# Optimization experiments

Measured on AMD Instinct MI355X. Metric: run time of the kernel, lower is better.

Reference implementation:

```python
import jax, jax.numpy as jnp
import numpy as np

B, L, D, H, R = 2, 2048, 1024, 16, 32
DH = D // H
LORA_SCALE = 64.0 / 32.0  # alpha / rank


def _ln(x, w, b):
    mu = jnp.mean(x, axis=-1, keepdims=True)
    xc = x - mu
    var = jnp.mean(xc * xc, axis=-1, keepdims=True)
    y = xc * jax.lax.rsqrt(var + 1e-5) * w
    return y + b if b is not None else y


def _rotate_half(x):
    x1, x2 = jnp.split(x, 2, axis=-1)
    return jnp.concatenate([-x2, x1], axis=-1)


def _apply_rotary(q, k):
    # q, k: [B, L, H, DH]
    seqlen = q.shape[1]
    inv_freq = 1.0 / (10000.0 ** (jnp.arange(0, DH, 2, dtype=jnp.float32) / DH))
    t = jnp.arange(seqlen, dtype=jnp.float32)
    freqs = t[:, None] * inv_freq[None, :]           # [L, DH/2]
    emb = jnp.concatenate([freqs, freqs], axis=-1)   # [L, DH]
    cos = jnp.cos(emb)[None, :, None, :]
    sin = jnp.sin(emb)[None, :, None, :]
    q = q * cos + _rotate_half(q) * sin
    k = k * cos + _rotate_half(k) * sin
    return q, k


def setup_inputs() -> dict:
    key = jax.random.key(0)
    ks = jax.random.split(key, 10)
    s = 0.02
    return {
        "x": jax.random.normal(ks[0], (B, L, D), dtype=jnp.float32),
        "seq_id": jnp.sort(jax.random.randint(ks[1], (B, L), 0, 4), axis=-1),
        "ln_w": jnp.ones((D,), jnp.float32),
        "ln_b": jnp.zeros((D,), jnp.float32),
        "w_qkv": jax.random.normal(ks[2], (3 * D, D), jnp.float32) * s,
        "q_lora_a": jax.random.normal(ks[3], (R, D), jnp.float32) * s,
        "q_lora_b": jax.random.normal(ks[4], (D, R), jnp.float32) * s,
        "v_lora_a": jax.random.normal(ks[5], (R, D), jnp.float32) * s,
        "v_lora_b": jax.random.normal(ks[6], (D, R), jnp.float32) * s,
        "q_ln_w": jnp.ones((D,), jnp.float32),
        "k_ln_w": jnp.ones((D,), jnp.float32),
        "w_out": jax.random.normal(ks[7], (D, D), jnp.float32) * s,
    }


def reference(x, seq_id, ln_w, ln_b, w_qkv, q_lora_a, q_lora_b,
              v_lora_a, v_lora_b, q_ln_w, k_ln_w, w_out):
    h = _ln(x, ln_w, ln_b)                          # [B, L, D]
    qkv = jnp.einsum('bld,ed->ble', h, w_qkv)       # [B, L, 3D]
    q, k, v = jnp.split(qkv, 3, axis=-1)
    q = q + LORA_SCALE * jnp.einsum('blr,dr->bld', jnp.einsum('bld,rd->blr', h, q_lora_a), q_lora_b)
    v = v + LORA_SCALE * jnp.einsum('blr,dr->bld', jnp.einsum('bld,rd->blr', h, v_lora_a), v_lora_b)
    q = _ln(q, q_ln_w, None)
    k = _ln(k, k_ln_w, None)
    q = q.reshape(B, L, H, DH)
    k = k.reshape(B, L, H, DH)
    q, k = _apply_rotary(q, k)
    qh = q.transpose(0, 2, 1, 3)                    # [B, H, L, DH]
    kh = k.transpose(0, 2, 1, 3)
    vh = v.reshape(B, L, H, DH).transpose(0, 2, 1, 3)
    scale = 1.0 / np.sqrt(DH)
    scores = jnp.einsum('bhqd,bhkd->bhqk', qh, kh) * scale
    mask = (seq_id[:, None, :, None] == seq_id[:, None, None, :])  # [B,1,L,L]
    scores = jnp.where(mask, scores, jnp.finfo(scores.dtype).min)
    attn = jax.nn.softmax(scores, axis=-1)
    ctx = jnp.einsum('bhqk,bhkd->bhqd', attn, vh)   # [B, H, L, DH]
    ctx = ctx.transpose(0, 2, 1, 3).reshape(B, L, D)
    return jnp.einsum('bld,ed->ble', ctx, w_out)
```

## Files before the change

kernel.cpp:

```cpp
#include <hip/hip_runtime.h>
#include <hip/hip_bf16.h>
#include <cmath>

constexpr int Bb = 2;
constexpr int Ls = 2048;
constexpr int Dd = 1024;
constexpr int Hh = 16;
constexpr int DHh = 64;
constexpr int Rr = 32;
constexpr int BL = Bb * Ls;
constexpr float LORA_SCALE = 2.0f;
constexpr float LN_EPS = 1e-5f;
constexpr float ATTN_SCALE = 0.125f;
constexpr float LOG2E = 1.4426950408889634f;
constexpr float QSCL = ATTN_SCALE * LOG2E;

typedef __attribute__((ext_vector_type(8))) short bf16x8;
typedef __attribute__((ext_vector_type(4))) float f32x4;

__device__ __forceinline__ unsigned short f2bf(float f) {
    __hip_bfloat16 b = __float2bfloat16(f);
    return *reinterpret_cast<unsigned short*>(&b);
}
__device__ __forceinline__ float bf2f(unsigned short u) {
    unsigned int x = ((unsigned int)u) << 16;
    return __uint_as_float(x);
}
__device__ __forceinline__ void async_copy16(const void* g, void* l) {
    __builtin_amdgcn_global_load_lds(
        (__attribute__((address_space(1))) void*)(void*)(size_t)g,
        (__attribute__((address_space(3))) void*)l, 16, 0, 0);
}

__device__ __forceinline__ float block_sum_256(float v, float* red) {
#pragma unroll
    for (int o = 32; o > 0; o >>= 1) v += __shfl_down(v, o, 64);
    const int lane = threadIdx.x & 63;
    const int wid = threadIdx.x >> 6;
    if (lane == 0) red[wid] = v;
    __syncthreads();
    float s = red[0] + red[1] + red[2] + red[3];
    __syncthreads();
    return s;
}

__global__ __launch_bounds__(256) void prep_ln_kernel(const float* __restrict__ w,
                                                      const float* __restrict__ qa,
                                                      const float* __restrict__ qb,
                                                      const float* __restrict__ va,
                                                      const float* __restrict__ vb,
                                                      const float* __restrict__ wout,
                                                      const float* __restrict__ x,
                                                      const float* __restrict__ lnw,
                                                      const float* __restrict__ lnb,
                                                      unsigned short* __restrict__ wqkvb,
                                                      unsigned short* __restrict__ woutb,
                                                      float* __restrict__ ropec,
                                                      float* __restrict__ ropes,
                                                      unsigned short* __restrict__ hb) {
    const int blk = blockIdx.x;
    const int tid = threadIdx.x;
    if (blk < 3 * Dd) {
        const int e = blk;
        const int d0 = tid * 4;
        __shared__ float br[Rr];
        const bool isq = (e < Dd);
        const bool isv = (e >= 2 * Dd);
        const float* bsrc = isq ? (qb + (size_t)e * Rr)
                                : (isv ? (vb + (size_t)(e - 2 * Dd) * Rr) : nullptr);
        const float* asrc = isq ? qa : va;
        if (bsrc && tid < Rr) br[tid] = bsrc[tid];
        __syncthreads();
        float acc[4] = {0.f, 0.f, 0.f, 0.f};
        if (bsrc) {
#pragma unroll 8
            for (int r = 0; r < Rr; ++r) {
                float4 av = *(const float4*)(asrc + (size_t)r * Dd + d0);
                acc[0] += br[r] * av.x; acc[1] += br[r] * av.y;
                acc[2] += br[r] * av.z; acc[3] += br[r] * av.w;
            }
        }
        float4 wv = *(const float4*)(w + (size_t)e * Dd + d0);
        ushort4 o;
        o.x = f2bf(wv.x + LORA_SCALE * acc[0]);
        o.y = f2bf(wv.y + LORA_SCALE * acc[1]);
        o.z = f2bf(wv.z + LORA_SCALE * acc[2]);
        o.w = f2bf(wv.w + LORA_SCALE * acc[3]);
        *(ushort4*)(wqkvb + (size_t)e * Dd + d0) = o;
    } else if (blk < 4 * Dd) {
        int i = ((blk - 3 * Dd) * 256 + tid) * 4;
        float4 v = *(const float4*)(wout + i);
        ushort4 o;
        o.x = f2bf(v.x); o.y = f2bf(v.y); o.z = f2bf(v.z); o.w = f2bf(v.w);
        *(ushort4*)(woutb + i) = o;
    } else if (blk < 4 * Dd + 256) {
        int i = (blk - 4 * Dd) * 256 + tid;
        int l = i >> 5;
        int f = i & 31;
        float invf = powf(10000.0f, -(float)f * (1.0f / 32.0f));
        float ang = (float)l * invf;
        float s, c;
        sincosf(ang, &s, &c);
        ropec[i] = c;
        ropes[i] = s;
    } else {
        const int w64 = tid >> 6;
        const int L = tid & 63;
        const int row = (blk - (4 * Dd + 256)) * 4 + w64;
        const float* xr = x + (size_t)row * Dd;
        float4 v4[4];
        float v[16];
#pragma unroll
        for (int c = 0; c < 4; ++c) {
            v4[c] = *(const float4*)(xr + c * 256 + L * 4);
            v[c * 4 + 0] = v4[c].x; v[c * 4 + 1] = v4[c].y;
            v[c * 4 + 2] = v4[c].z; v[c * 4 + 3] = v4[c].w;
        }
        float s = 0.f;
#pragma unroll
        for (int j = 0; j < 16; ++j) s += v[j];
#pragma unroll
        for (int off = 1; off < 64; off <<= 1) s += __shfl_xor(s, off, 64);
        float mean = s * (1.0f / Dd);
        float sq = 0.f;
#pragma unroll
        for (int j = 0; j < 16; ++j) {
            v[j] -= mean;
            sq += v[j] * v[j];
        }
#pragma unroll
        for (int off = 1; off < 64; off <<= 1) sq += __shfl_xor(sq, off, 64);
        float rs = rsqrtf(sq * (1.0f / Dd) + LN_EPS);
        unsigned short* hr = hb + (size_t)row * Dd;
#pragma unroll
        for (int c = 0; c < 4; ++c) {
            int d = c * 256 + L * 4;
            float4 wv = *(const float4*)(lnw + d);
            float4 bv = *(const float4*)(lnb + d);
            ushort4 o;
            o.x = f2bf(v[c * 4 + 0] * rs * wv.x + bv.x);
            o.y = f2bf(v[c * 4 + 1] * rs * wv.y + bv.y);
            o.z = f2bf(v[c * 4 + 2] * rs * wv.z + bv.z);
            o.w = f2bf(v[c * 4 + 3] * rs * wv.w + bv.w);
            *(ushort4*)(hr + d) = o;
        }
    }
}

__global__ __launch_bounds__(256) void gemm_bt_mfma(const unsigned short* __restrict__ A,
                                                    const unsigned short* __restrict__ B,
                                                    unsigned short* __restrict__ C,
                                                    int M, int N, int K) {
    __shared__ short As[128 * 64];
    __shared__ short Bs[128 * 64];
    const int tid = threadIdx.x;
    const int w = tid >> 6, lane = tid & 63, quad = lane >> 4, l15 = lane & 15;
    const int m0 = blockIdx.y * 128, n0 = blockIdx.x * 128;
    const int wm = (w & 1) * 64, wn = (w >> 1) * 64;
    f32x4 acc[4][4];
#pragma unroll
    for (int i = 0; i < 4; ++i)
#pragma unroll
        for (int j = 0; j < 4; ++j) acc[i][j] = f32x4{0.f, 0.f, 0.f, 0.f};

    for (int k0 = 0; k0 < K; k0 += 64) {
#pragma unroll
        for (int j = 0; j < 4; ++j) {
            int c = tid + j * 256;
            int row = c >> 3;
            int jg = (c & 7) ^ (row & 7);
            async_copy16(A + (size_t)(m0 + row) * K + k0 + jg * 8, As + c * 8);
        }
#pragma unroll
        for (int j = 0; j < 4; ++j) {
            int c = tid + j * 256;
            int row = c >> 3;
            int jg = (c & 7) ^ (row & 7);
            async_copy16(B + (size_t)(n0 + row) * K + k0 + jg * 8, Bs + c * 8);
        }
        __syncthreads();
#pragma unroll
        for (int ks = 0; ks < 2; ++ks) {
            bf16x8 a[4], b[4];
#pragma unroll
            for (int mi = 0; mi < 4; ++mi) {
                int row = wm + mi * 16 + l15;
                int ch = (ks * 4 + quad) ^ (row & 7);
                a[mi] = *(const bf16x8*)&As[row * 64 + ch * 8];
            }
#pragma unroll
            for (int ni = 0; ni < 4; ++ni) {
                int row = wn + ni * 16 + l15;
                int ch = (ks * 4 + quad) ^ (row & 7);
                b[ni] = *(const bf16x8*)&Bs[row * 64 + ch * 8];
            }
#pragma unroll
            for (int mi = 0; mi < 4; ++mi)
#pragma unroll
                for (int ni = 0; ni < 4; ++ni)
                    acc[mi][ni] = __builtin_amdgcn_mfma_f32_16x16x32_bf16(a[mi], b[ni], acc[mi][ni], 0, 0, 0);
        }
        __syncthreads();
    }
#pragma unroll
    for (int mi = 0; mi < 4; ++mi)
#pragma unroll
        for (int ni = 0; ni < 4; ++ni)
#pragma unroll
            for (int r = 0; r < 4; ++r)
                C[(size_t)(m0 + wm + mi * 16 + quad * 4 + r) * N + n0 + wn + ni * 16 + l15] =
                    f2bf(acc[mi][ni][r]);
}

__global__ __launch_bounds__(256) void gemm_bt_mfma_n64(const unsigned short* __restrict__ A,
                                                        const unsigned short* __restrict__ B,
                                                        float* __restrict__ C,
                                                        int M, int N, int K) {
    __shared__ short As[128 * 64];
    __shared__ short Bs[64 * 64];
    const int tid = threadIdx.x;
    const int w = tid >> 6, lane = tid & 63, quad = lane >> 4, l15 = lane & 15;
    const int m0 = blockIdx.y * 128, n0 = blockIdx.x * 64;
    const int wm = (w & 1) * 64, wn = (w >> 1) * 32;
    f32x4 acc[4][2];
#pragma unroll
    for (int i = 0; i < 4; ++i)
#pragma unroll
        for (int j = 0; j < 2; ++j) acc[i][j] = f32x4{0.f, 0.f, 0.f, 0.f};

    for (int k0 = 0; k0 < K; k0 += 64) {
#pragma unroll
        for (int j = 0; j < 4; ++j) {
            int c = tid + j * 256;
            int row = c >> 3;
            int jg = (c & 7) ^ (row & 7);
            async_copy16(A + (size_t)(m0 + row) * K + k0 + jg * 8, As + c * 8);
        }
#pragma unroll
        for (int j = 0; j < 2; ++j) {
            int c = tid + j * 256;
            int row = c >> 3;
            int jg = (c & 7) ^ (row & 7);
            async_copy16(B + (size_t)(n0 + row) * K + k0 + jg * 8, Bs + c * 8);
        }
        __syncthreads();
#pragma unroll
        for (int ks = 0; ks < 2; ++ks) {
            bf16x8 a[4], b[2];
#pragma unroll
            for (int mi = 0; mi < 4; ++mi) {
                int row = wm + mi * 16 + l15;
                int ch = (ks * 4 + quad) ^ (row & 7);
                a[mi] = *(const bf16x8*)&As[row * 64 + ch * 8];
            }
#pragma unroll
            for (int ni = 0; ni < 2; ++ni) {
                int row = wn + ni * 16 + l15;
                int ch = (ks * 4 + quad) ^ (row & 7);
                b[ni] = *(const bf16x8*)&Bs[row * 64 + ch * 8];
            }
#pragma unroll
            for (int mi = 0; mi < 4; ++mi)
#pragma unroll
                for (int ni = 0; ni < 2; ++ni)
                    acc[mi][ni] = __builtin_amdgcn_mfma_f32_16x16x32_bf16(a[mi], b[ni], acc[mi][ni], 0, 0, 0);
        }
        __syncthreads();
    }
#pragma unroll
    for (int mi = 0; mi < 4; ++mi)
#pragma unroll
        for (int ni = 0; ni < 2; ++ni)
#pragma unroll
            for (int r = 0; r < 4; ++r)
                C[(size_t)(m0 + wm + mi * 16 + quad * 4 + r) * N + n0 + wn + ni * 16 + l15] =
                    acc[mi][ni][r];
}

__global__ __launch_bounds__(256) void qkv_final_kernel(const unsigned short* __restrict__ qkvb,
                                                        const float* __restrict__ qlnw,
                                                        const float* __restrict__ klnw,
                                                        const float* __restrict__ ropec,
                                                        const float* __restrict__ ropes,
                                                        unsigned short* __restrict__ qt,
                                                        unsigned short* __restrict__ kt,
                                                        unsigned short* __restrict__ vtt) {
    const int blk = blockIdx.x;
    const int tid = threadIdx.x;
    if (blk < BL / 4) {
        const int w64 = tid >> 6;
        const int L = tid & 63;
        const int row = blk * 4 + w64;
        const int b = row >> 11;
        const int l = row & (Ls - 1);
        const unsigned short* qp = qkvb + (size_t)row * (3 * Dd);
        const unsigned short* kp = qp + Dd;

        bf16x8 qA = *(const bf16x8*)(qp + L * 8);
        bf16x8 qB = *(const bf16x8*)(qp + 512 + L * 8);
        bf16x8 kA = *(const bf16x8*)(kp + L * 8);
        bf16x8 kB = *(const bf16x8*)(kp + 512 + L * 8);
        float vq[16], vk[16];
#pragma unroll
        for (int j = 0; j < 8; ++j) {
            vq[j] = bf2f((unsigned short)qA[j]);
            vq[8 + j] = bf2f((unsigned short)qB[j]);
            vk[j] = bf2f((unsigned short)kA[j]);
            vk[8 + j] = bf2f((unsigned short)kB[j]);
        }
        float sq = 0.f, sk = 0.f;
#pragma unroll
        for (int j = 0; j < 16; ++j) { sq += vq[j]; sk += vk[j]; }
#pragma unroll
        for (int off = 1; off < 64; off <<= 1) {
            sq += __shfl_xor(sq, off, 64);
            sk += __shfl_xor(sk, off, 64);
        }
        float mq = sq * (1.0f / Dd), mk = sk * (1.0f / Dd);
        float vvq = 0.f, vvk = 0.f;
#pragma unroll
        for (int j = 0; j < 16; ++j) {
            vq[j] -= mq; vvq += vq[j] * vq[j];
            vk[j] -= mk; vvk += vk[j] * vk[j];
        }
#pragma unroll
        for (int off = 1; off < 64; off <<= 1) {
            vvq += __shfl_xor(vvq, off, 64);
            vvk += __shfl_xor(vvk, off, 64);
        }
        float rsq = rsqrtf(vvq * (1.0f / Dd) + LN_EPS);
        float rsk = rsqrtf(vvk * (1.0f / Dd) + LN_EPS);

        float yq[16], yk[16];
        {
            float4 w0 = *(const float4*)(qlnw + L * 8);
            float4 w1 = *(const float4*)(qlnw + L * 8 + 4);
            float4 w2 = *(const float4*)(qlnw + 512 + L * 8);
            float4 w3 = *(const float4*)(qlnw + 512 + L * 8 + 4);
            const float* wp = (const float*)&w0;
            yq[0] = vq[0] * rsq * w0.x; yq[1] = vq[1] * rsq * w0.y;
            yq[2] = vq[2] * rsq * w0.z; yq[3] = vq[3] * rsq * w0.w;
            yq[4] = vq[4] * rsq * w1.x; yq[5] = vq[5] * rsq * w1.y;
            yq[6] = vq[6] * rsq * w1.z; yq[7] = vq[7] * rsq * w1.w;
            yq[8] = vq[8] * rsq * w2.x; yq[9] = vq[9] * rsq * w2.y;
            yq[10] = vq[10] * rsq * w2.z; yq[11] = vq[11] * rsq * w2.w;
            yq[12] = vq[12] * rsq * w3.x; yq[13] = vq[13] * rsq * w3.y;
            yq[14] = vq[14] * rsq * w3.z; yq[15] = vq[15] * rsq * w3.w;
            (void)wp;
        }
        {
            float4 w0 = *(const float4*)(klnw + L * 8);
            float4 w1 = *(const float4*)(klnw + L * 8 + 4);
            float4 w2 = *(const float4*)(klnw + 512 + L * 8);
            float4 w3 = *(const float4*)(klnw + 512 + L * 8 + 4);
            yk[0] = vk[0] * rsk * w0.x; yk[1] = vk[1] * rsk * w0.y;
            yk[2] = vk[2] * rsk * w0.z; yk[3] = vk[3] * rsk * w0.w;
            yk[4] = vk[4] * rsk * w1.x; yk[5] = vk[5] * rsk * w1.y;
            yk[6] = vk[6] * rsk * w1.z; yk[7] = vk[7] * rsk * w1.w;
            yk[8] = vk[8] * rsk * w2.x; yk[9] = vk[9] * rsk * w2.y;
            yk[10] = vk[10] * rsk * w2.z; yk[11] = vk[11] * rsk * w2.w;
            yk[12] = vk[12] * rsk * w3.x; yk[13] = vk[13] * rsk * w3.y;
            yk[14] = vk[14] * rsk * w3.z; yk[15] = vk[15] * rsk * w3.w;
        }

        float cs[8], sn[8];
        {
            int fbase = l * 32 + (L & 3) * 8;
            float4 c0 = *(const float4*)(ropec + fbase);
            float4 c1 = *(const float4*)(ropec + fbase + 4);
            float4 s0 = *(const float4*)(ropes + fbase);
            float4 s1 = *(const float4*)(ropes + fbase + 4);
            cs[0] = c0.x; cs[1] = c0.y; cs[2] = c0.z; cs[3] = c0.w;
            cs[4] = c1.x; cs[5] = c1.y; cs[6] = c1.z; cs[7] = c1.w;
            sn[0] = s0.x; sn[1] = s0.y; sn[2] = s0.z; sn[3] = s0.w;
            sn[4] = s1.x; sn[5] = s1.y; sn[6] = s1.z; sn[7] = s1.w;
        }
        const float sgn = (L & 4) ? 1.0f : -1.0f;
        ushort4 oqA0, oqA1, oqB0, oqB1, okA0, okA1, okB0, okB1;
        unsigned short* pqA = (unsigned short*)&oqA0;
        unsigned short outqA[8], outqB[8], outkA[8], outkB[8];
#pragma unroll
        for (int j = 0; j < 8; ++j) {
            float pA = __shfl_xor(yq[j], 4, 64);
            float pB = __shfl_xor(yq[8 + j], 4, 64);
            outqA[j] = f2bf((yq[j] * cs[j] + sgn * pA * sn[j]) * QSCL);
            outqB[j] = f2bf((yq[8 + j] * cs[j] + sgn * pB * sn[j]) * QSCL);
            float pkA = __shfl_xor(yk[j], 4, 64);
            float pkB = __shfl_xor(yk[8 + j], 4, 64);
            outkA[j] = f2bf(yk[j] * cs[j] + sgn * pkA * sn[j]);
            outkB[j] = f2bf(yk[8 + j] * cs[j] + sgn * pkB * sn[j]);
        }
        (void)pqA; (void)oqA1; (void)oqB0; (void)oqB1; (void)okA0; (void)okA1; (void)okB0; (void)okB1;
        const int hA = L >> 3;
        const int dh0 = (L & 7) * 8;
        size_t offA = (((size_t)(b * Hh + hA)) * Ls + l) * DHh + dh0;
        size_t offB = (((size_t)(b * Hh + 8 + hA)) * Ls + l) * DHh + dh0;
        *(uint4*)(qt + offA) = *(uint4*)outqA;
        *(uint4*)(qt + offB) = *(uint4*)outqB;
        *(uint4*)(kt + offA) = *(uint4*)outkA;
        *(uint4*)(kt + offB) = *(uint4*)outkB;
    } else {
        const int t2 = blk - BL / 4;
        const int l0 = (t2 & 31) * 64;
        const int h = (t2 >> 5) & 15;
        const int b = t2 >> 9;
        __shared__ short t[64][72];
        const unsigned short* src = qkvb + (size_t)b * Ls * (3 * Dd) + 2 * Dd + h * 64;
#pragma unroll
        for (int j = 0; j < 2; ++j) {
            int g = tid + j * 256;
            int row = g >> 3;
            int c0 = (g & 7) * 8;
            uint4 vv = *(const uint4*)(src + (size_t)(l0 + row) * (3 * Dd) + c0);
            *(uint4*)&t[row][c0] = vv;
        }
        __syncthreads();
        unsigned short* dst = vtt + ((size_t)(b * Hh + h) * DHh) * Ls;
#pragma unroll
        for (int j = 0; j < 2; ++j) {
            int g = tid + j * 256;
            int dh = g >> 3;
            int lc = (g & 7) * 8;
            ushort4 o0, o1;
            unsigned short* p0 = (unsigned short*)&o0;
            unsigned short* p1 = (unsigned short*)&o1;
#pragma unroll
            for (int i = 0; i < 4; ++i) p0[i] = (unsigned short)t[lc + i][dh];
#pragma unroll
            for (int i = 0; i < 4; ++i) p1[i] = (unsigned short)t[lc + 4 + i][dh];
            *(ushort4*)(dst + (size_t)dh * Ls + l0 + lc) = o0;
            *(ushort4*)(dst + (size_t)dh * Ls + l0 + lc + 4) = o1;
        }
    }
}

constexpr int PSP = 76;

__global__ __launch_bounds__(256) void attn_kernel(const unsigned short* __restrict__ qt,
                                                   const unsigned short* __restrict__ kt,
                                                   const unsigned short* __restrict__ vtt,
                                                   const int* __restrict__ seq_id,
                                                   unsigned short* __restrict__ ctxb) {
    const int id = blockIdx.x;
    const int c8 = id & 7;
    const int x = (id >> 3) & 15;
    const int g4 = id >> 7;
    const int v = c8 + 8 * g4;
    const int b = v >> 4;
    const int h = v & 15;
    const int q0 = x * 128;

    const size_t base = ((size_t)(b * Hh + h)) * Ls * DHh;
    const size_t base_v = ((size_t)(b * Hh + h)) * DHh * Ls;
    const int* sid = seq_id + (size_t)b * Ls;

    __shared__ short Ks[64 * 64];
    __shared__ short Vs[64 * 64];
    __shared__ short Ps[8][16 * PSP];
    __shared__ int sq_s[128];

    const int tid = threadIdx.x;
    const int w = tid >> 6;
    const int lane = tid & 63;
    const int quad = lane >> 4;
    const int l15 = lane & 15;

    if (tid < 128) sq_s[tid] = sid[q0 + tid];
    const int qmin = sid[q0];
    const int qmax = sid[q0 + 127];

    bf16x8 a0[2], a1[2];
#pragma unroll
    for (int sub = 0; sub < 2; ++sub) {
        int qrow = q0 + sub * 64 + w * 16 + l15;
        a0[sub] = *(const bf16x8*)(qt + base + (size_t)qrow * DHh + quad * 8);
        a1[sub] = *(const bf16x8*)(qt + base + (size_t)qrow * DHh + 32 + quad * 8);
    }

    bool need = false;
    if (lane < 32) {
        int kmn = sid[lane * 64];
        int kmx = sid[lane * 64 + 63];
        need = (kmn <= qmax) && (kmx >= qmin);
    }
    unsigned long long bmask = __ballot(need);
    const int t0 = __builtin_ctzll(bmask);
    const int t1 = 64 - __builtin_clzll(bmask);

    float lsum[2][4] = {{0.f, 0.f, 0.f, 0.f}, {0.f, 0.f, 0.f, 0.f}};
    f32x4 O[2][4];
#pragma unroll
    for (int sub = 0; sub < 2; ++sub)
#pragma unroll
        for (int r = 0; r < 4; ++r) O[sub][r] = f32x4{0.f, 0.f, 0.f, 0.f};

    for (int t = t0; t < t1; ++t) {
        const int k0 = t * 64;
        __syncthreads();
#pragma unroll
        for (int j = 0; j < 2; ++j) {
            int cc = tid + j * 256;
            int row = cc >> 3;
            int jg = (cc & 7) ^ (row & 7);
            async_copy16(kt + base + (size_t)(k0 + row) * DHh + jg * 8, &Ks[cc * 8]);
            async_copy16(vtt + base_v + (size_t)row * Ls + k0 + jg * 8, &Vs[cc * 8]);
        }
        __syncthreads();

        f32x4 s[2][4];
#pragma unroll
        for (int kg = 0; kg < 4; ++kg) {
            int krow = kg * 16 + l15;
            bf16x8 b0 = *(const bf16x8*)&Ks[krow * 64 + ((0 + quad) ^ (krow & 7)) * 8];
            bf16x8 b1 = *(const bf16x8*)&Ks[krow * 64 + ((4 + quad) ^ (krow & 7)) * 8];
#pragma unroll
            for (int sub = 0; sub < 2; ++sub) {
                f32x4 acc = {0.f, 0.f, 0.f, 0.f};
                acc = __builtin_amdgcn_mfma_f32_16x16x32_bf16(a0[sub], b0, acc, 0, 0, 0);
                acc = __builtin_amdgcn_mfma_f32_16x16x32_bf16(a1[sub], b1, acc, 0, 0, 0);
                s[sub][kg] = acc;
            }
        }
        const int kmn = sid[k0];
        const int kmx = sid[k0 + 63];
        const bool nomask = (kmn == kmx) && (qmin == qmax) && (kmn == qmin);
        if (!nomask) {
#pragma unroll
            for (int sub = 0; sub < 2; ++sub) {
                int sqv[4];
#pragma unroll
                for (int r = 0; r < 4; ++r) sqv[r] = sq_s[sub * 64 + w * 16 + quad * 4 + r];
#pragma unroll
                for (int kg = 0; kg < 4; ++kg) {
                    int skv = sid[k0 + kg * 16 + l15];
#pragma unroll
                    for (int r = 0; r < 4; ++r)
                        if (sqv[r] != skv) s[sub][kg][r] = -3.0e38f;
                }
            }
        }
#pragma unroll
        for (int sub = 0; sub < 2; ++sub) {
#pragma unroll
            for (int kg = 0; kg < 4; ++kg)
#pragma unroll
                for (int r = 0; r < 4; ++r)
                    s[sub][kg][r] = __builtin_amdgcn_exp2f(s[sub][kg][r]);
#pragma unroll
            for (int r = 0; r < 4; ++r)
                lsum[sub][r] += s[sub][0][r] + s[sub][1][r] + s[sub][2][r] + s[sub][3][r];
#pragma unroll
            for (int kg = 0; kg < 4; ++kg)
#pragma unroll
                for (int r = 0; r < 4; ++r)
                    Ps[w * 2 + sub][(quad * 4 + r) * PSP + kg * 16 + l15] =
                        (short)f2bf(s[sub][kg][r]);
        }
        bf16x8 pa0[2], pa1[2];
#pragma unroll
        for (int sub = 0; sub < 2; ++sub) {
            pa0[sub] = *(const bf16x8*)&Ps[w * 2 + sub][l15 * PSP + quad * 8];
            pa1[sub] = *(const bf16x8*)&Ps[w * 2 + sub][l15 * PSP + 32 + quad * 8];
        }
#pragma unroll
        for (int ng = 0; ng < 4; ++ng) {
            int vrow = ng * 16 + l15;
            bf16x8 vb0 = *(const bf16x8*)&Vs[vrow * 64 + ((0 + quad) ^ (vrow & 7)) * 8];
            bf16x8 vb1 = *(const bf16x8*)&Vs[vrow * 64 + ((4 + quad) ^ (vrow & 7)) * 8];
#pragma unroll
            for (int sub = 0; sub < 2; ++sub) {
                O[sub][ng] = __builtin_amdgcn_mfma_f32_16x16x32_bf16(pa0[sub], vb0, O[sub][ng], 0, 0, 0);
                O[sub][ng] = __builtin_amdgcn_mfma_f32_16x16x32_bf16(pa1[sub], vb1, O[sub][ng], 0, 0, 0);
            }
        }
    }

#pragma unroll
    for (int sub = 0; sub < 2; ++sub) {
#pragma unroll
        for (int off = 1; off < 16; off <<= 1)
#pragma unroll
            for (int r = 0; r < 4; ++r)
                lsum[sub][r] += __shfl_xor(lsum[sub][r], off, 64);
        float inv_l[4];
#pragma unroll
        for (int r = 0; r < 4; ++r) inv_l[r] = 1.0f / lsum[sub][r];
#pragma unroll
        for (int ng = 0; ng < 4; ++ng)
#pragma unroll
            for (int r = 0; r < 4; ++r) {
                int q = q0 + sub * 64 + w * 16 + quad * 4 + r;
                ctxb[((size_t)b * Ls + q) * Dd + h * DHh + ng * 16 + l15] =
                    f2bf(O[sub][ng][r] * inv_l[r]);
            }
    }
}

extern "C" void kernel_launch(void* const* d_in, const int* in_sizes, int n_in,
                              void* d_out, int out_size, void* d_ws, size_t ws_size,
                              hipStream_t stream) {
    const float* x = (const float*)d_in[0];
    const int* seq_id = (const int*)d_in[1];
    const float* ln_w = (const float*)d_in[2];
    const float* ln_b = (const float*)d_in[3];
    const float* w_qkv = (const float*)d_in[4];
    const float* q_lora_a = (const float*)d_in[5];
    const float* q_lora_b = (const float*)d_in[6];
    const float* v_lora_a = (const float*)d_in[7];
    const float* v_lora_b = (const float*)d_in[8];
    const float* q_ln_w = (const float*)d_in[9];
    const float* k_ln_w = (const float*)d_in[10];
    const float* w_out = (const float*)d_in[11];
    float* out = (float*)d_out;

    const size_t SZ = (size_t)BL * Dd;
    float* p = (float*)d_ws;
    float* ropec = p;          p += (size_t)Ls * 32;
    float* ropes = p;          p += (size_t)Ls * 32;
    unsigned short* ub = (unsigned short*)p;
    unsigned short* qkvb = ub; ub += 3 * SZ;
    unsigned short* hb = ub;   ub += SZ;
    unsigned short* qt = ub;   ub += SZ;
    unsigned short* kt = ub;   ub += SZ;
    unsigned short* vtt = ub;  ub += SZ;
    unsigned short* ctxb = ub; ub += SZ;
    unsigned short* wqkvb = ub; ub += (size_t)3 * Dd * Dd;
    unsigned short* woutb = ub; ub += (size_t)Dd * Dd;

    prep_ln_kernel<<<4 * Dd + 256 + BL / 4, 256, 0, stream>>>(
        w_qkv, q_lora_a, q_lora_b, v_lora_a, v_lora_b, w_out,
        x, ln_w, ln_b, wqkvb, woutb, ropec, ropes, hb);
    {
        dim3 g(3 * Dd / 128, BL / 128);
        gemm_bt_mfma<<<g, 256, 0, stream>>>(hb, wqkvb, qkvb, BL, 3 * Dd, Dd);
    }
    qkv_final_kernel<<<BL / 4 + 1024, 256, 0, stream>>>(qkvb, q_ln_w, k_ln_w,
                                                        ropec, ropes, qt, kt, vtt);
    attn_kernel<<<512, 256, 0, stream>>>(qt, kt, vtt, seq_id, ctxb);
    {
        dim3 g(Dd / 64, BL / 128);
        gemm_bt_mfma_n64<<<g, 256, 0, stream>>>(ctxb, woutb, out, BL, Dd, Dd);
    }
}
```

Measured before the change: 208.0 us.

## Halve attention query tile and load K/V fragments directly from global memory

The attention kernel now handles 64 query rows per block instead of 128 and launches twice as many blocks. K and V fragments are read straight from global memory into registers instead of being staged through shared memory with async copies. This removes the two block-wide barriers per key tile and cuts LDS use, which should raise occupancy and parallelism. In exchange, each K/V tile is now re-read once per wave and block, so global and L2 traffic goes up and the loads are no longer coalesced or swizzled.

```diff
diff --git a/kernel.cpp b/kernel.cpp
--- a/kernel.cpp
+++ b/kernel.cpp
@@ -443,21 +443,19 @@
                                                    unsigned short* __restrict__ ctxb) {
     const int id = blockIdx.x;
     const int c8 = id & 7;
-    const int x = (id >> 3) & 15;
-    const int g4 = id >> 7;
+    const int x = (id >> 3) & 31;
+    const int g4 = id >> 8;
     const int v = c8 + 8 * g4;
     const int b = v >> 4;
     const int h = v & 15;
-    const int q0 = x * 128;
+    const int q0 = x * 64;
 
     const size_t base = ((size_t)(b * Hh + h)) * Ls * DHh;
     const size_t base_v = ((size_t)(b * Hh + h)) * DHh * Ls;
     const int* sid = seq_id + (size_t)b * Ls;
 
-    __shared__ short Ks[64 * 64];
-    __shared__ short Vs[64 * 64];
-    __shared__ short Ps[8][16 * PSP];
-    __shared__ int sq_s[128];
+    __shared__ short Ps[4][16 * PSP];
+    __shared__ int sq_s[64];
 
     const int tid = threadIdx.x;
     const int w = tid >> 6;
@@ -465,17 +463,18 @@
     const int quad = lane >> 4;
     const int l15 = lane & 15;
 
-    if (tid < 128) sq_s[tid] = sid[q0 + tid];
+    if (tid < 64) sq_s[tid] = sid[q0 + tid];
+    __syncthreads();
     const int qmin = sid[q0];
-    const int qmax = sid[q0 + 127];
-
-    bf16x8 a0[2], a1[2];
-#pragma unroll
-    for (int sub = 0; sub < 2; ++sub) {
-        int qrow = q0 + sub * 64 + w * 16 + l15;
-        a0[sub] = *(const bf16x8*)(qt + base + (size_t)qrow * DHh + quad * 8);
-        a1[sub] = *(const bf16x8*)(qt + base + (size_t)qrow * DHh + 32 + quad * 8);
-    }
+    const int qmax = sid[q0 + 63];
+
+    const int qrow = q0 + w * 16 + l15;
+    const bf16x8 a0 = *(const bf16x8*)(qt + base + (size_t)qrow * DHh + quad * 8);
+    const bf16x8 a1 = *(const bf16x8*)(qt + base + (size_t)qrow * DHh + 32 + quad * 8);
+
+    int sqv[4];
+#pragma unroll
+    for (int r = 0; r < 4; ++r) sqv[r] = sq_s[w * 16 + quad * 4 + r];
 
     bool need = false;
     if (lane < 32) {
@@ -487,113 +486,86 @@
     const int t0 = __builtin_ctzll(bmask);
     const int t1 = 64 - __builtin_clzll(bmask);
 
-    float lsum[2][4] = {{0.f, 0.f, 0.f, 0.f}, {0.f, 0.f, 0.f, 0.f}};
-    f32x4 O[2][4];
-#pragma unroll
-    for (int sub = 0; sub < 2; ++sub)
-#pragma unroll
-        for (int r = 0; r < 4; ++r) O[sub][r] = f32x4{0.f, 0.f, 0.f, 0.f};
+    float lsum[4] = {0.f, 0.f, 0.f, 0.f};
+    f32x4 O[4];
+#pragma unroll
+    for (int r = 0; r < 4; ++r) O[r] = f32x4{0.f, 0.f, 0.f, 0.f};
 
     for (int t = t0; t < t1; ++t) {
         const int k0 = t * 64;
-        __syncthreads();
-#pragma unroll
-        for (int j = 0; j < 2; ++j) {
-            int cc = tid + j * 256;
-            int row = cc >> 3;
-            int jg = (cc & 7) ^ (row & 7);
-            async_copy16(kt + base + (size_t)(k0 + row) * DHh + jg * 8, &Ks[cc * 8]);
-            async_copy16(vtt + base_v + (size_t)row * Ls + k0 + jg * 8, &Vs[cc * 8]);
-        }
-        __syncthreads();
-
-        f32x4 s[2][4];
+
+        bf16x8 vb0[4], vb1[4];
+#pragma unroll
+        for (int ng = 0; ng < 4; ++ng) {
+            const unsigned short* vp = vtt + base_v + (size_t)(ng * 16 + l15) * Ls + k0;
+            vb0[ng] = *(const bf16x8*)(vp + quad * 8);
+            vb1[ng] = *(const bf16x8*)(vp + 32 + quad * 8);
+        }
+
+        f32x4 s[4];
 #pragma unroll
         for (int kg = 0; kg < 4; ++kg) {
-            int krow = kg * 16 + l15;
-            bf16x8 b0 = *(const bf16x8*)&Ks[krow * 64 + ((0 + quad) ^ (krow & 7)) * 8];
-            bf16x8 b1 = *(const bf16x8*)&Ks[krow * 64 + ((4 + quad) ^ (krow & 7)) * 8];
-#pragma unroll
-            for (int sub = 0; sub < 2; ++sub) {
-                f32x4 acc = {0.f, 0.f, 0.f, 0.f};
-                acc = __builtin_amdgcn_mfma_f32_16x16x32_bf16(a0[sub], b0, acc, 0, 0, 0);
-                acc = __builtin_amdgcn_mfma_f32_16x16x32_bf16(a1[sub], b1, acc, 0, 0, 0);
-                s[sub][kg] = acc;
-            }
-        }
+            const unsigned short* kp = kt + base + (size_t)(k0 + kg * 16 + l15) * DHh;
+            bf16x8 b0 = *(const bf16x8*)(kp + quad * 8);
+            bf16x8 b1 = *(const bf16x8*)(kp + 32 + quad * 8);
+            f32x4 acc = {0.f, 0.f, 0.f, 0.f};
+            acc = __builtin_amdgcn_mfma_f32_16x16x32_bf16(a0, b0, acc, 0, 0, 0);
+            acc = __builtin_amdgcn_mfma_f32_16x16x32_bf16(a1, b1, acc, 0, 0, 0);
+            s[kg] = acc;
+        }
+
         const int kmn = sid[k0];
         const int kmx = sid[k0 + 63];
         const bool nomask = (kmn == kmx) && (qmin == qmax) && (kmn == qmin);
         if (!nomask) {
 #pragma unroll
-            for (int sub = 0; sub < 2; ++sub) {
-                int sqv[4];
-#pragma unroll
-                for (int r = 0; r < 4; ++r) sqv[r] = sq_s[sub * 64 + w * 16 + quad * 4 + r];
-#pragma unroll
-                for (int kg = 0; kg < 4; ++kg) {
-                    int skv = sid[k0 + kg * 16 + l15];
-#pragma unroll
-                    for (int r = 0; r < 4; ++r)
-                        if (sqv[r] != skv) s[sub][kg][r] = -3.0e38f;
-                }
+            for (int kg = 0; kg < 4; ++kg) {
+                int skv = sid[k0 + kg * 16 + l15];
+#pragma unroll
+                for (int r = 0; r < 4; ++r)
+                    if (sqv[r] != skv) s[kg][r] = -3.0e38f;
             }
         }
 #pragma unroll
-        for (int sub = 0; sub < 2; ++sub) {
-#pragma unroll
-            for (int kg = 0; kg < 4; ++kg)
-#pragma unroll
-                for (int r = 0; r < 4; ++r)
-                    s[sub][kg][r] = __builtin_amdgcn_exp2f(s[sub][kg][r]);
+        for (int kg = 0; kg < 4; ++kg)
 #pragma unroll
             for (int r = 0; r < 4; ++r)
-                lsum[sub][r] += s[sub][0][r] + s[sub][1][r] + s[sub][2][r] + s[sub][3][r];
-#pragma unroll
-            for (int kg = 0; kg < 4; ++kg)
-#pragma unroll
-                for (int r = 0; r < 4; ++r)
-                    Ps[w * 2 + sub][(quad * 4 + r) * PSP + kg * 16 + l15] =
-                        (short)f2bf(s[sub][kg][r]);
-        }
-        bf16x8 pa0[2], pa1[2];
-#pragma unroll
-        for (int sub = 0; sub < 2; ++sub) {
-            pa0[sub] = *(const bf16x8*)&Ps[w * 2 + sub][l15 * PSP + quad * 8];
-            pa1[sub] = *(const bf16x8*)&Ps[w * 2 + sub][l15 * PSP + 32 + quad * 8];
-        }
+                s[kg][r] = __builtin_amdgcn_exp2f(s[kg][r]);
+#pragma unroll
+        for (int r = 0; r < 4; ++r)
+            lsum[r] += s[0][r] + s[1][r] + s[2][r] + s[3][r];
+
+#pragma unroll
+        for (int kg = 0; kg < 4; ++kg)
+#pragma unroll
+            for (int r = 0; r < 4; ++r)
+                Ps[w][(quad * 4 + r) * PSP + kg * 16 + l15] = (short)f2bf(s[kg][r]);
+
+        bf16x8 pa0 = *(const bf16x8*)&Ps[w][l15 * PSP + quad * 8];
+        bf16x8 pa1 = *(const bf16x8*)&Ps[w][l15 * PSP + 32 + quad * 8];
 #pragma unroll
         for (int ng = 0; ng < 4; ++ng) {
-            int vrow = ng * 16 + l15;
-            bf16x8 vb0 = *(const bf16x8*)&Vs[vrow * 64 + ((0 + quad) ^ (vrow & 7)) * 8];
-            bf16x8 vb1 = *(const bf16x8*)&Vs[vrow * 64 + ((4 + quad) ^ (vrow & 7)) * 8];
-#pragma unroll
-            for (int sub = 0; sub < 2; ++sub) {
-                O[sub][ng] = __builtin_amdgcn_mfma_f32_16x16x32_bf16(pa0[sub], vb0, O[sub][ng], 0, 0, 0);
-                O[sub][ng] = __builtin_amdgcn_mfma_f32_16x16x32_bf16(pa1[sub], vb1, O[sub][ng], 0, 0, 0);
-            }
-        }
-    }
-
-#pragma unroll
-    for (int sub = 0; sub < 2; ++sub) {
-#pragma unroll
-        for (int off = 1; off < 16; off <<= 1)
-#pragma unroll
-            for (int r = 0; r < 4; ++r)
-                lsum[sub][r] += __shfl_xor(lsum[sub][r], off, 64);
-        float inv_l[4];
-#pragma unroll
-        for (int r = 0; r < 4; ++r) inv_l[r] = 1.0f / lsum[sub][r];
-#pragma unroll
-        for (int ng = 0; ng < 4; ++ng)
-#pragma unroll
-            for (int r = 0; r < 4; ++r) {
-                int q = q0 + sub * 64 + w * 16 + quad * 4 + r;
-                ctxb[((size_t)b * Ls + q) * Dd + h * DHh + ng * 16 + l15] =
-                    f2bf(O[sub][ng][r] * inv_l[r]);
-            }
-    }
+            O[ng] = __builtin_amdgcn_mfma_f32_16x16x32_bf16(pa0, vb0[ng], O[ng], 0, 0, 0);
+            O[ng] = __builtin_amdgcn_mfma_f32_16x16x32_bf16(pa1, vb1[ng], O[ng], 0, 0, 0);
+        }
+    }
+
+#pragma unroll
+    for (int off = 1; off < 16; off <<= 1)
+#pragma unroll
+        for (int r = 0; r < 4; ++r)
+            lsum[r] += __shfl_xor(lsum[r], off, 64);
+    float inv_l[4];
+#pragma unroll
+    for (int r = 0; r < 4; ++r) inv_l[r] = 1.0f / lsum[r];
+#pragma unroll
+    for (int ng = 0; ng < 4; ++ng)
+#pragma unroll
+        for (int r = 0; r < 4; ++r) {
+            int q = q0 + w * 16 + quad * 4 + r;
+            ctxb[((size_t)b * Ls + q) * Dd + h * DHh + ng * 16 + l15] =
+                f2bf(O[ng][r] * inv_l[r]);
+        }
 }
 
 extern "C" void kernel_launch(void* const* d_in, const int* in_sizes, int n_in,
@@ -636,7 +608,7 @@
     }
     qkv_final_kernel<<<BL / 4 + 1024, 256, 0, stream>>>(qkvb, q_ln_w, k_ln_w,
                                                         ropec, ropes, qt, kt, vtt);
-    attn_kernel<<<512, 256, 0, stream>>>(qt, kt, vtt, seq_id, ctxb);
+    attn_kernel<<<1024, 256, 0, stream>>>(qt, kt, vtt, seq_id, ctxb);
     {
         dim3 g(Dd / 64, BL / 128);
         gemm_bt_mfma_n64<<<g, 256, 0, stream>>>(ctxb, woutb, out, BL, Dd, Dd);
```

New measurement: 285.2 us. 37.1% more time.

## Double-buffer K/V tiles in attention and prefetch the next tile

Applied to the files above, without the earlier changes.

The attention loop now keeps two LDS buffers each for K and V. It issues the asynchronous global-to-LDS copy for the next key tile before computing on the current one, so each iteration needs one barrier instead of two. The per-row query seq ids are loaded into registers once before the loop, and the key seq ids are loaded at the top of each iteration. Both MFMA sections are wrapped in s_setprio raises, and some unused helper code and dead variables are removed. The cost is twice the LDS for K/V, which may reduce occupancy.

```diff
diff --git a/kernel.cpp b/kernel.cpp
--- a/kernel.cpp
+++ b/kernel.cpp
@@ -30,18 +30,6 @@
     __builtin_amdgcn_global_load_lds(
         (__attribute__((address_space(1))) void*)(void*)(size_t)g,
         (__attribute__((address_space(3))) void*)l, 16, 0, 0);
-}
-
-__device__ __forceinline__ float block_sum_256(float v, float* red) {
-#pragma unroll
-    for (int o = 32; o > 0; o >>= 1) v += __shfl_down(v, o, 64);
-    const int lane = threadIdx.x & 63;
-    const int wid = threadIdx.x >> 6;
-    if (lane == 0) red[wid] = v;
-    __syncthreads();
-    float s = red[0] + red[1] + red[2] + red[3];
-    __syncthreads();
-    return s;
 }
 
 __global__ __launch_bounds__(256) void prep_ln_kernel(const float* __restrict__ w,
@@ -337,7 +325,6 @@
             float4 w1 = *(const float4*)(qlnw + L * 8 + 4);
             float4 w2 = *(const float4*)(qlnw + 512 + L * 8);
             float4 w3 = *(const float4*)(qlnw + 512 + L * 8 + 4);
-            const float* wp = (const float*)&w0;
             yq[0] = vq[0] * rsq * w0.x; yq[1] = vq[1] * rsq * w0.y;
             yq[2] = vq[2] * rsq * w0.z; yq[3] = vq[3] * rsq * w0.w;
             yq[4] = vq[4] * rsq * w1.x; yq[5] = vq[5] * rsq * w1.y;
@@ -346,7 +333,6 @@
             yq[10] = vq[10] * rsq * w2.z; yq[11] = vq[11] * rsq * w2.w;
             yq[12] = vq[12] * rsq * w3.x; yq[13] = vq[13] * rsq * w3.y;
             yq[14] = vq[14] * rsq * w3.z; yq[15] = vq[15] * rsq * w3.w;
-            (void)wp;
         }
         {
             float4 w0 = *(const float4*)(klnw + L * 8);
@@ -376,8 +362,6 @@
             sn[4] = s1.x; sn[5] = s1.y; sn[6] = s1.z; sn[7] = s1.w;
         }
         const float sgn = (L & 4) ? 1.0f : -1.0f;
-        ushort4 oqA0, oqA1, oqB0, oqB1, okA0, okA1, okB0, okB1;
-        unsigned short* pqA = (unsigned short*)&oqA0;
         unsigned short outqA[8], outqB[8], outkA[8], outkB[8];
 #pragma unroll
         for (int j = 0; j < 8; ++j) {
@@ -390,7 +374,6 @@
             outkA[j] = f2bf(yk[j] * cs[j] + sgn * pkA * sn[j]);
             outkB[j] = f2bf(yk[8 + j] * cs[j] + sgn * pkB * sn[j]);
         }
-        (void)pqA; (void)oqA1; (void)oqB0; (void)oqB1; (void)okA0; (void)okA1; (void)okB0; (void)okB1;
         const int hA = L >> 3;
         const int dh0 = (L & 7) * 8;
         size_t offA = (((size_t)(b * Hh + hA)) * Ls + l) * DHh + dh0;
@@ -454,8 +437,8 @@
     const size_t base_v = ((size_t)(b * Hh + h)) * DHh * Ls;
     const int* sid = seq_id + (size_t)b * Ls;
 
-    __shared__ short Ks[64 * 64];
-    __shared__ short Vs[64 * 64];
+    __shared__ short Ks[2][64 * 64];
+    __shared__ short Vs[2][64 * 64];
     __shared__ short Ps[8][16 * PSP];
     __shared__ int sq_s[128];
 
@@ -469,14 +452,6 @@
     const int qmin = sid[q0];
     const int qmax = sid[q0 + 127];
 
-    bf16x8 a0[2], a1[2];
-#pragma unroll
-    for (int sub = 0; sub < 2; ++sub) {
-        int qrow = q0 + sub * 64 + w * 16 + l15;
-        a0[sub] = *(const bf16x8*)(qt + base + (size_t)qrow * DHh + quad * 8);
-        a1[sub] = *(const bf16x8*)(qt + base + (size_t)qrow * DHh + 32 + quad * 8);
-    }
-
     bool need = false;
     if (lane < 32) {
         int kmn = sid[lane * 64];
@@ -487,32 +462,60 @@
     const int t0 = __builtin_ctzll(bmask);
     const int t1 = 64 - __builtin_clzll(bmask);
 
-    float lsum[2][4] = {{0.f, 0.f, 0.f, 0.f}, {0.f, 0.f, 0.f, 0.f}};
-    f32x4 O[2][4];
-#pragma unroll
-    for (int sub = 0; sub < 2; ++sub)
-#pragma unroll
-        for (int r = 0; r < 4; ++r) O[sub][r] = f32x4{0.f, 0.f, 0.f, 0.f};
-
-    for (int t = t0; t < t1; ++t) {
-        const int k0 = t * 64;
-        __syncthreads();
+    auto stage = [&](int buf, int t) {
 #pragma unroll
         for (int j = 0; j < 2; ++j) {
             int cc = tid + j * 256;
             int row = cc >> 3;
             int jg = (cc & 7) ^ (row & 7);
-            async_copy16(kt + base + (size_t)(k0 + row) * DHh + jg * 8, &Ks[cc * 8]);
-            async_copy16(vtt + base_v + (size_t)row * Ls + k0 + jg * 8, &Vs[cc * 8]);
-        }
-        __syncthreads();
+            async_copy16(kt + base + (size_t)(t * 64 + row) * DHh + jg * 8,
+                         &Ks[buf][cc * 8]);
+            async_copy16(vtt + base_v + (size_t)row * Ls + t * 64 + jg * 8,
+                         &Vs[buf][cc * 8]);
+        }
+    };
+
+    stage(0, t0);
+    bf16x8 a0[2], a1[2];
+#pragma unroll
+    for (int sub = 0; sub < 2; ++sub) {
+        int qrow = q0 + sub * 64 + w * 16 + l15;
+        a0[sub] = *(const bf16x8*)(qt + base + (size_t)qrow * DHh + quad * 8);
+        a1[sub] = *(const bf16x8*)(qt + base + (size_t)qrow * DHh + 32 + quad * 8);
+    }
+
+    int sqv[2][4];
+    float lsum[2][4] = {{0.f, 0.f, 0.f, 0.f}, {0.f, 0.f, 0.f, 0.f}};
+    f32x4 O[2][4];
+#pragma unroll
+    for (int sub = 0; sub < 2; ++sub)
+#pragma unroll
+        for (int r = 0; r < 4; ++r) O[sub][r] = f32x4{0.f, 0.f, 0.f, 0.f};
+
+    __syncthreads();
+#pragma unroll
+    for (int sub = 0; sub < 2; ++sub)
+#pragma unroll
+        for (int r = 0; r < 4; ++r) sqv[sub][r] = sq_s[sub * 64 + w * 16 + quad * 4 + r];
+
+    for (int t = t0; t < t1; ++t) {
+        const int cur = (t - t0) & 1;
+        if (t + 1 < t1) stage(cur ^ 1, t + 1);
+        const int k0 = t * 64;
+
+        int skv[4];
+#pragma unroll
+        for (int kg = 0; kg < 4; ++kg) skv[kg] = sid[k0 + kg * 16 + l15];
+        const int kmn = sid[k0];
+        const int kmx = sid[k0 + 63];
 
         f32x4 s[2][4];
+        __builtin_amdgcn_s_setprio(1);
 #pragma unroll
         for (int kg = 0; kg < 4; ++kg) {
             int krow = kg * 16 + l15;
-            bf16x8 b0 = *(const bf16x8*)&Ks[krow * 64 + ((0 + quad) ^ (krow & 7)) * 8];
-            bf16x8 b1 = *(const bf16x8*)&Ks[krow * 64 + ((4 + quad) ^ (krow & 7)) * 8];
+            bf16x8 b0 = *(const bf16x8*)&Ks[cur][krow * 64 + ((0 + quad) ^ (krow & 7)) * 8];
+            bf16x8 b1 = *(const bf16x8*)&Ks[cur][krow * 64 + ((4 + quad) ^ (krow & 7)) * 8];
 #pragma unroll
             for (int sub = 0; sub < 2; ++sub) {
                 f32x4 acc = {0.f, 0.f, 0.f, 0.f};
@@ -521,23 +524,17 @@
                 s[sub][kg] = acc;
             }
         }
-        const int kmn = sid[k0];
-        const int kmx = sid[k0 + 63];
+        __builtin_amdgcn_s_setprio(0);
+
         const bool nomask = (kmn == kmx) && (qmin == qmax) && (kmn == qmin);
         if (!nomask) {
 #pragma unroll
-            for (int sub = 0; sub < 2; ++sub) {
-                int sqv[4];
-#pragma unroll
-                for (int r = 0; r < 4; ++r) sqv[r] = sq_s[sub * 64 + w * 16 + quad * 4 + r];
-#pragma unroll
-                for (int kg = 0; kg < 4; ++kg) {
-                    int skv = sid[k0 + kg * 16 + l15];
+            for (int sub = 0; sub < 2; ++sub)
+#pragma unroll
+                for (int kg = 0; kg < 4; ++kg)
 #pragma unroll
                     for (int r = 0; r < 4; ++r)
-                        if (sqv[r] != skv) s[sub][kg][r] = -3.0e38f;
-                }
-            }
+                        if (sqv[sub][r] != skv[kg]) s[sub][kg][r] = -3.0e38f;
         }
 #pragma unroll
         for (int sub = 0; sub < 2; ++sub) {
@@ -556,23 +553,28 @@
                     Ps[w * 2 + sub][(quad * 4 + r) * PSP + kg * 16 + l15] =
                         (short)f2bf(s[sub][kg][r]);
         }
+
         bf16x8 pa0[2], pa1[2];
 #pragma unroll
         for (int sub = 0; sub < 2; ++sub) {
             pa0[sub] = *(const bf16x8*)&Ps[w * 2 + sub][l15 * PSP + quad * 8];
             pa1[sub] = *(const bf16x8*)&Ps[w * 2 + sub][l15 * PSP + 32 + quad * 8];
         }
+        __builtin_amdgcn_s_setprio(1);
 #pragma unroll
         for (int ng = 0; ng < 4; ++ng) {
             int vrow = ng * 16 + l15;
-            bf16x8 vb0 = *(const bf16x8*)&Vs[vrow * 64 + ((0 + quad) ^ (vrow & 7)) * 8];
-            bf16x8 vb1 = *(const bf16x8*)&Vs[vrow * 64 + ((4 + quad) ^ (vrow & 7)) * 8];
+            bf16x8 vb0 = *(const bf16x8*)&Vs[cur][vrow * 64 + ((0 + quad) ^ (vrow & 7)) * 8];
+            bf16x8 vb1 = *(const bf16x8*)&Vs[cur][vrow * 64 + ((4 + quad) ^ (vrow & 7)) * 8];
 #pragma unroll
             for (int sub = 0; sub < 2; ++sub) {
                 O[sub][ng] = __builtin_amdgcn_mfma_f32_16x16x32_bf16(pa0[sub], vb0, O[sub][ng], 0, 0, 0);
                 O[sub][ng] = __builtin_amdgcn_mfma_f32_16x16x32_bf16(pa1[sub], vb1, O[sub][ng], 0, 0, 0);
             }
         }
+        __builtin_amdgcn_s_setprio(0);
+
+        __syncthreads();
     }
 
 #pragma unroll
```

Measured after the change: 206.7 us. No clear change (-0.6%).
